# Performance work log

Hardware: AMD Instinct MI355X
Metric: run time of the kernel (lower is better)

The kernel has to match this reference:

```python
import jax, jax.numpy as jnp
import numpy as np

B, C, H, W = 16, 96, 64, 64
N = H * W
BN = B * N
K = 16  # neighbors per node
E = BN * K
C_OUT = 96


def setup_inputs() -> dict:
    key = jax.random.key(0)
    k1, k2, k3, k4 = jax.random.split(key, 4)
    x = jax.random.normal(k1, (B, C, H, W), dtype=jnp.float32)
    # KNN-style edge list over flat node ids (node = b*N + n):
    # every node appears K times as a target (row 0), random sources (row 1).
    dst = jnp.repeat(jnp.arange(BN, dtype=jnp.int64), K)
    src = jax.random.randint(k2, (E,), 0, BN, dtype=jnp.int64)
    edge_index = jnp.stack([dst, src], axis=0)
    Wc = jax.random.normal(k3, (C_OUT, 2 * C), dtype=jnp.float32) * 0.05
    bc = jax.random.normal(k4, (C_OUT,), dtype=jnp.float32) * 0.05
    return {"x": x, "edge_index": edge_index, "Wc": Wc, "bc": bc}


def reference(x, edge_index, Wc, bc):
    b, c, h, w = x.shape
    n = h * w
    # Flatten to node features [B*N, C] with node id = b*N + n
    feats = x.reshape(b, c, n).transpose(0, 2, 1).reshape(b * n, c)
    # Max-relative aggregation: gather, subtract, scatter-max over targets
    diff = feats[edge_index[1]] - feats[edge_index[0]]        # [E, C]
    agg = jax.ops.segment_max(diff, edge_index[0], num_segments=b * n)  # [BN, C]
    x_j = agg.reshape(b, n, c).transpose(0, 2, 1)             # [B, C, N]
    x_n = x.reshape(b, c, n)                                   # [B, C, N]
    # Interleaved channel concat: (x_0, xj_0, x_1, xj_1, ...) -> [B, 2C, N]
    cat = jnp.stack([x_n, x_j], axis=2).reshape(b, 2 * c, n)
    # BasicConv: 1x1 conv (GEMM over channels) + bias + ReLU
    out = jnp.einsum('oc,bcn->bon', Wc, cat) + bc[None, :, None]
    out = jax.nn.relu(out)
    return out.reshape(b, -1, h, w)
```

## Files before the change

kernel.cpp:

```cpp
#include <hip/hip_runtime.h>

#define B_   16
#define C_   96
#define N_   4096
#define BN_  65536
#define K_   16
#define E_   (BN_ * K_)

typedef __attribute__((ext_vector_type(8))) short bf16x8;
typedef __attribute__((ext_vector_type(4))) float f32x4;

union FragU { uint32_t u[4]; bf16x8 v; };

__device__ __forceinline__ uint32_t pack2_bf16(float a, float b) {
    uint32_t ua = __builtin_bit_cast(uint32_t, a);
    uint32_t ub = __builtin_bit_cast(uint32_t, b);
    ua = (ua + 0x7fffu + ((ua >> 16) & 1u)) >> 16;
    ub = (ub + 0x7fffu + ((ub >> 16) & 1u)) >> 16;
    return (ua & 0xffffu) | (ub << 16);
}
__device__ __forceinline__ float lo16f(uint32_t u) {
    return __builtin_bit_cast(float, u << 16);
}
__device__ __forceinline__ float hi16f(uint32_t u) {
    return __builtin_bit_cast(float, u & 0xffff0000u);
}

__global__ __launch_bounds__(256) void transpose_k(const float* __restrict__ x,
                                                   ushort* __restrict__ feats_bf) {
    __shared__ float tile[32][65];
    int b  = blockIdx.z;
    int c0 = blockIdx.y * 32;
    int n0 = blockIdx.x * 64;
    const float* xp = x + (size_t)b * C_ * N_;
    for (int t = threadIdx.x; t < 32 * 64; t += 256) {
        int c = t >> 6, n = t & 63;
        tile[c][n] = xp[(size_t)(c0 + c) * N_ + n0 + n];
    }
    __syncthreads();
    ushort* fp = feats_bf + ((size_t)b * N_ + n0) * C_ + c0;
    for (int t = threadIdx.x; t < 64 * 16; t += 256) {
        int n = t >> 4, cq = t & 15;
        uint32_t p = pack2_bf16(tile[2 * cq][n], tile[2 * cq + 1][n]);
        *(uint32_t*)(fp + (size_t)n * C_ + 2 * cq) = p;
    }
}

__global__ __launch_bounds__(256) void gather_max_k(const ushort* __restrict__ feats,
                                                    const int* __restrict__ src,
                                                    ushort* __restrict__ agg_bf) {
    int tid = threadIdx.x;
    int ln  = tid >> 3;
    int r   = tid & 7;
    size_t i = (size_t)blockIdx.x * 32 + ln;
    const int* s = src + i * K_;

    float m[12];
#pragma unroll
    for (int j = 0; j < 12; j++) m[j] = -3.0e38f;

#pragma unroll
    for (int q = 0; q < 4; q++) {
        int4 iv = ((const int4*)s)[q];
        int ids[4] = {iv.x, iv.y, iv.z, iv.w};
#pragma unroll
        for (int kk = 0; kk < 4; kk++) {
            const uint2* row = (const uint2*)(feats + (size_t)ids[kk] * C_);
#pragma unroll
            for (int j = 0; j < 3; j++) {
                uint2 v = row[r + 8 * j];
                m[4 * j + 0] = fmaxf(m[4 * j + 0], lo16f(v.x));
                m[4 * j + 1] = fmaxf(m[4 * j + 1], hi16f(v.x));
                m[4 * j + 2] = fmaxf(m[4 * j + 2], lo16f(v.y));
                m[4 * j + 3] = fmaxf(m[4 * j + 3], hi16f(v.y));
            }
        }
    }

    const uint2* own = (const uint2*)(feats + i * (size_t)C_);
    ushort* ap = agg_bf + i * (size_t)C_;
#pragma unroll
    for (int j = 0; j < 3; j++) {
        uint2 o = own[r + 8 * j];
        uint2 p;
        p.x = pack2_bf16(m[4 * j + 0] - lo16f(o.x), m[4 * j + 1] - hi16f(o.x));
        p.y = pack2_bf16(m[4 * j + 2] - lo16f(o.y), m[4 * j + 3] - hi16f(o.y));
        *(uint2*)(ap + (size_t)(r + 8 * j) * 4) = p;
    }
}

__global__ __launch_bounds__(256) void pack_w_k(const float* __restrict__ Wc,
                                                ushort* __restrict__ Wp) {
    int t = blockIdx.x * 256 + threadIdx.x;
    if (t >= 36 * 64) return;
    int fid = t >> 6, l = t & 63;
    int ks = fid / 6, to = fid % 6;
    int o = to * 16 + (l & 15), g = l >> 4;
    uint32_t packed[4];
#pragma unroll
    for (int h = 0; h < 4; h++) {
        int e0 = 2 * h, e1 = 2 * h + 1;
        int k0 = ks * 32 + 4 * g + (e0 & 3) + 16 * (e0 >> 2);
        int k1 = ks * 32 + 4 * g + (e1 & 3) + 16 * (e1 >> 2);
        int ko0 = (k0 < 96) ? 2 * k0 : 2 * (k0 - 96) + 1;
        int ko1 = (k1 < 96) ? 2 * k1 : 2 * (k1 - 96) + 1;
        packed[h] = pack2_bf16(Wc[(size_t)o * 192 + ko0], Wc[(size_t)o * 192 + ko1]);
    }
    uint4 u = make_uint4(packed[0], packed[1], packed[2], packed[3]);
    ((uint4*)Wp)[t] = u;
}

__global__ __launch_bounds__(256) void conv_mfma_k(const ushort* __restrict__ feats_bf,
                                                   const ushort* __restrict__ agg_bf,
                                                   const ushort* __restrict__ Wp,
                                                   const float* __restrict__ bc,
                                                   float* __restrict__ out) {
    __shared__ ushort A_lds[128 * 200];
    int tid = threadIdx.x;
    int w = tid >> 6, l = tid & 63;
    int blk = blockIdx.x;
    int b = blk >> 5;
    int n0 = (blk & 31) << 7;

    float bcr[6];
#pragma unroll
    for (int to = 0; to < 6; to++) bcr[to] = bc[to * 16 + (l & 15)];

    const ushort* fb = feats_bf + ((size_t)b * N_ + n0) * C_;
#pragma unroll
    for (int i = 0; i < 12; i++) {
        int tau = i * 256 + tid;
        int n = tau / 24;
        int q = tau - n * 24;
        uint2 p = *(const uint2*)(fb + (size_t)n * C_ + 4 * q);
        int idx = n * 200 + ((4 * q) ^ ((n & 15) << 2));
        *(uint2*)&A_lds[idx] = p;
    }
    const ushort* ab = agg_bf + ((size_t)b * N_ + n0) * C_;
#pragma unroll
    for (int i = 0; i < 12; i++) {
        int tau = i * 256 + tid;
        int n = tau / 24;
        int q = tau - n * 24;
        uint2 p = *(const uint2*)(ab + (size_t)n * C_ + 4 * q);
        int idx = n * 200 + ((96 + 4 * q) ^ ((n & 15) << 2));
        *(uint2*)&A_lds[idx] = p;
    }
    __syncthreads();

    f32x4 acc[2][6];
#pragma unroll
    for (int tm = 0; tm < 2; tm++)
#pragma unroll
        for (int to = 0; to < 6; to++)
            acc[tm][to] = (f32x4){0.f, 0.f, 0.f, 0.f};

    const uint4* wp4 = (const uint4*)Wp;
    int g = l >> 4;
    int m = (l & 15) << 2;

#pragma unroll
    for (int ks = 0; ks < 6; ks++) {
        FragU bfrag[6];
#pragma unroll
        for (int to = 0; to < 6; to++) {
            uint4 u = wp4[(ks * 6 + to) * 64 + l];
            bfrag[to].u[0] = u.x; bfrag[to].u[1] = u.y;
            bfrag[to].u[2] = u.z; bfrag[to].u[3] = u.w;
        }
        FragU afrag[2];
#pragma unroll
        for (int tm = 0; tm < 2; tm++) {
            int n = w * 32 + tm * 16 + (l & 15);
            int base = n * 200;
            int k1 = ks * 32 + 4 * g;
            uint2 lo = *(const uint2*)&A_lds[base + (k1 ^ m)];
            uint2 hi = *(const uint2*)&A_lds[base + ((k1 + 16) ^ m)];
            afrag[tm].u[0] = lo.x; afrag[tm].u[1] = lo.y;
            afrag[tm].u[2] = hi.x; afrag[tm].u[3] = hi.y;
        }
#pragma unroll
        for (int tm = 0; tm < 2; tm++)
#pragma unroll
            for (int to = 0; to < 6; to++)
                acc[tm][to] = __builtin_amdgcn_mfma_f32_16x16x32_bf16(
                    afrag[tm].v, bfrag[to].v, acc[tm][to], 0, 0, 0);
    }

    __syncthreads();
    float* OT = (float*)A_lds;
#pragma unroll
    for (int tm = 0; tm < 2; tm++)
#pragma unroll
        for (int to = 0; to < 6; to++) {
            int o = to * 16 + (l & 15);
#pragma unroll
            for (int reg = 0; reg < 4; reg++) {
                int nl = w * 32 + tm * 16 + ((l >> 4) << 2) + reg;
                OT[o * 132 + nl] = fmaxf(acc[tm][to][reg] + bcr[to], 0.0f);
            }
        }
    __syncthreads();

#pragma unroll
    for (int i = 0; i < 12; i++) {
        int f = i * 256 + tid;
        int o = f >> 5, c4 = f & 31;
        float4 v = *(const float4*)&OT[o * 132 + 4 * c4];
        *(float4*)(out + ((size_t)b * C_ + o) * N_ + n0 + 4 * c4) = v;
    }
}

extern "C" void kernel_launch(void* const* d_in, const int* in_sizes, int n_in,
                              void* d_out, int out_size, void* d_ws, size_t ws_size,
                              hipStream_t stream) {
    const float* x   = (const float*)d_in[0];
    const int*   ei  = (const int*)d_in[1];
    const float* Wc  = (const float*)d_in[2];
    const float* bc  = (const float*)d_in[3];
    float* out = (float*)d_out;

    const int* src = ei + E_;

    ushort* feats_bf = (ushort*)d_ws;
    ushort* agg_bf   = (ushort*)((char*)d_ws + (size_t)BN_ * C_ * 2);
    ushort* Wp       = (ushort*)((char*)d_ws + (size_t)BN_ * C_ * 4);

    pack_w_k<<<9, 256, 0, stream>>>(Wc, Wp);

    dim3 gA(N_ / 64, C_ / 32, B_);
    transpose_k<<<gA, 256, 0, stream>>>(x, feats_bf);

    gather_max_k<<<BN_ / 32, 256, 0, stream>>>(feats_bf, src, agg_bf);

    conv_mfma_k<<<B_ * (N_ / 128), 256, 0, stream>>>(feats_bf, agg_bf, Wp, bc, out);
}
```

Baseline: 59.20 us.

## Fold weight packing into gather kernel and simplify conv epilogue with 512 threads

The weight-packing kernel is merged into the gather-max launch as 9 extra tail blocks, which removes one kernel launch. The conv kernel moves to 512 threads with one 16-row M tile per wave. It loads its feature and aggregate tiles with 16-byte loads into an equivalent XOR-swizzled LDS layout. Its output is now written straight from registers as float4 stores, skipping the LDS transpose and two barriers, at the cost of less coalesced global writes (16-byte pieces strided by N).

```diff
diff --git a/kernel.cpp b/kernel.cpp
--- a/kernel.cpp
+++ b/kernel.cpp
@@ -48,8 +48,31 @@
 
 __global__ __launch_bounds__(256) void gather_max_k(const ushort* __restrict__ feats,
                                                     const int* __restrict__ src,
-                                                    ushort* __restrict__ agg_bf) {
+                                                    ushort* __restrict__ agg_bf,
+                                                    const float* __restrict__ Wc,
+                                                    ushort* __restrict__ Wp) {
     int tid = threadIdx.x;
+    if (blockIdx.x >= 2048) {
+        int t = (blockIdx.x - 2048) * 256 + tid;
+        if (t >= 36 * 64) return;
+        int fid = t >> 6, l = t & 63;
+        int ks = fid / 6, to = fid % 6;
+        int o = to * 16 + (l & 15), g = l >> 4;
+        uint32_t packed[4];
+#pragma unroll
+        for (int h = 0; h < 4; h++) {
+            int e0 = 2 * h, e1 = 2 * h + 1;
+            int k0 = ks * 32 + 4 * g + (e0 & 3) + 16 * (e0 >> 2);
+            int k1 = ks * 32 + 4 * g + (e1 & 3) + 16 * (e1 >> 2);
+            int ko0 = (k0 < 96) ? 2 * k0 : 2 * (k0 - 96) + 1;
+            int ko1 = (k1 < 96) ? 2 * k1 : 2 * (k1 - 96) + 1;
+            packed[h] = pack2_bf16(Wc[(size_t)o * 192 + ko0],
+                                   Wc[(size_t)o * 192 + ko1]);
+        }
+        ((uint4*)Wp)[t] = make_uint4(packed[0], packed[1], packed[2], packed[3]);
+        return;
+    }
+
     int ln  = tid >> 3;
     int r   = tid & 7;
     size_t i = (size_t)blockIdx.x * 32 + ln;
@@ -89,28 +112,7 @@
     }
 }
 
-__global__ __launch_bounds__(256) void pack_w_k(const float* __restrict__ Wc,
-                                                ushort* __restrict__ Wp) {
-    int t = blockIdx.x * 256 + threadIdx.x;
-    if (t >= 36 * 64) return;
-    int fid = t >> 6, l = t & 63;
-    int ks = fid / 6, to = fid % 6;
-    int o = to * 16 + (l & 15), g = l >> 4;
-    uint32_t packed[4];
-#pragma unroll
-    for (int h = 0; h < 4; h++) {
-        int e0 = 2 * h, e1 = 2 * h + 1;
-        int k0 = ks * 32 + 4 * g + (e0 & 3) + 16 * (e0 >> 2);
-        int k1 = ks * 32 + 4 * g + (e1 & 3) + 16 * (e1 >> 2);
-        int ko0 = (k0 < 96) ? 2 * k0 : 2 * (k0 - 96) + 1;
-        int ko1 = (k1 < 96) ? 2 * k1 : 2 * (k1 - 96) + 1;
-        packed[h] = pack2_bf16(Wc[(size_t)o * 192 + ko0], Wc[(size_t)o * 192 + ko1]);
-    }
-    uint4 u = make_uint4(packed[0], packed[1], packed[2], packed[3]);
-    ((uint4*)Wp)[t] = u;
-}
-
-__global__ __launch_bounds__(256) void conv_mfma_k(const ushort* __restrict__ feats_bf,
+__global__ __launch_bounds__(512) void conv_mfma_k(const ushort* __restrict__ feats_bf,
                                                    const ushort* __restrict__ agg_bf,
                                                    const ushort* __restrict__ Wp,
                                                    const float* __restrict__ bc,
@@ -127,37 +129,30 @@
     for (int to = 0; to < 6; to++) bcr[to] = bc[to * 16 + (l & 15)];
 
     const ushort* fb = feats_bf + ((size_t)b * N_ + n0) * C_;
-#pragma unroll
-    for (int i = 0; i < 12; i++) {
-        int tau = i * 256 + tid;
+    const ushort* ab = agg_bf + ((size_t)b * N_ + n0) * C_;
+#pragma unroll
+    for (int i = 0; i < 6; i++) {
+        int tau = i * 512 + tid;
         int n = tau / 24;
-        int q = tau - n * 24;
-        uint2 p = *(const uint2*)(fb + (size_t)n * C_ + 4 * q);
-        int idx = n * 200 + ((4 * q) ^ ((n & 15) << 2));
-        *(uint2*)&A_lds[idx] = p;
-    }
-    const ushort* ab = agg_bf + ((size_t)b * N_ + n0) * C_;
-#pragma unroll
-    for (int i = 0; i < 12; i++) {
-        int tau = i * 256 + tid;
-        int n = tau / 24;
-        int q = tau - n * 24;
-        uint2 p = *(const uint2*)(ab + (size_t)n * C_ + 4 * q);
-        int idx = n * 200 + ((96 + 4 * q) ^ ((n & 15) << 2));
-        *(uint2*)&A_lds[idx] = p;
+        int p = tau - n * 24;
+        const ushort* srcp = (p < 12) ? (fb + (size_t)n * C_ + 8 * p)
+                                      : (ab + (size_t)n * C_ + 8 * (p - 12));
+        uint4 u = *(const uint4*)srcp;
+        if (n & 1) { uint32_t t0 = u.x, t1 = u.y; u.x = u.z; u.y = u.w; u.z = t0; u.w = t1; }
+        int slot = p ^ ((n >> 1) & 7);
+        *(uint4*)&A_lds[n * 200 + slot * 8] = u;
     }
     __syncthreads();
 
-    f32x4 acc[2][6];
-#pragma unroll
-    for (int tm = 0; tm < 2; tm++)
-#pragma unroll
-        for (int to = 0; to < 6; to++)
-            acc[tm][to] = (f32x4){0.f, 0.f, 0.f, 0.f};
+    f32x4 acc[6];
+#pragma unroll
+    for (int to = 0; to < 6; to++) acc[to] = (f32x4){0.f, 0.f, 0.f, 0.f};
 
     const uint4* wp4 = (const uint4*)Wp;
     int g = l >> 4;
     int m = (l & 15) << 2;
+    int nrow = w * 16 + (l & 15);
+    int abase = nrow * 200;
 
 #pragma unroll
     for (int ks = 0; ks < 6; ks++) {
@@ -168,46 +163,28 @@
             bfrag[to].u[0] = u.x; bfrag[to].u[1] = u.y;
             bfrag[to].u[2] = u.z; bfrag[to].u[3] = u.w;
         }
-        FragU afrag[2];
-#pragma unroll
-        for (int tm = 0; tm < 2; tm++) {
-            int n = w * 32 + tm * 16 + (l & 15);
-            int base = n * 200;
-            int k1 = ks * 32 + 4 * g;
-            uint2 lo = *(const uint2*)&A_lds[base + (k1 ^ m)];
-            uint2 hi = *(const uint2*)&A_lds[base + ((k1 + 16) ^ m)];
-            afrag[tm].u[0] = lo.x; afrag[tm].u[1] = lo.y;
-            afrag[tm].u[2] = hi.x; afrag[tm].u[3] = hi.y;
-        }
-#pragma unroll
-        for (int tm = 0; tm < 2; tm++)
-#pragma unroll
-            for (int to = 0; to < 6; to++)
-                acc[tm][to] = __builtin_amdgcn_mfma_f32_16x16x32_bf16(
-                    afrag[tm].v, bfrag[to].v, acc[tm][to], 0, 0, 0);
-    }
-
-    __syncthreads();
-    float* OT = (float*)A_lds;
-#pragma unroll
-    for (int tm = 0; tm < 2; tm++)
-#pragma unroll
-        for (int to = 0; to < 6; to++) {
-            int o = to * 16 + (l & 15);
-#pragma unroll
-            for (int reg = 0; reg < 4; reg++) {
-                int nl = w * 32 + tm * 16 + ((l >> 4) << 2) + reg;
-                OT[o * 132 + nl] = fmaxf(acc[tm][to][reg] + bcr[to], 0.0f);
-            }
-        }
-    __syncthreads();
-
-#pragma unroll
-    for (int i = 0; i < 12; i++) {
-        int f = i * 256 + tid;
-        int o = f >> 5, c4 = f & 31;
-        float4 v = *(const float4*)&OT[o * 132 + 4 * c4];
-        *(float4*)(out + ((size_t)b * C_ + o) * N_ + n0 + 4 * c4) = v;
+        int k1 = ks * 32 + 4 * g;
+        uint2 lo = *(const uint2*)&A_lds[abase + (k1 ^ m)];
+        uint2 hi = *(const uint2*)&A_lds[abase + ((k1 + 16) ^ m)];
+        FragU afrag;
+        afrag.u[0] = lo.x; afrag.u[1] = lo.y;
+        afrag.u[2] = hi.x; afrag.u[3] = hi.y;
+#pragma unroll
+        for (int to = 0; to < 6; to++)
+            acc[to] = __builtin_amdgcn_mfma_f32_16x16x32_bf16(
+                afrag.v, bfrag[to].v, acc[to], 0, 0, 0);
+    }
+
+    int nl = n0 + w * 16 + ((l >> 4) << 2);
+#pragma unroll
+    for (int to = 0; to < 6; to++) {
+        int o = to * 16 + (l & 15);
+        float4 v;
+        v.x = fmaxf(acc[to][0] + bcr[to], 0.0f);
+        v.y = fmaxf(acc[to][1] + bcr[to], 0.0f);
+        v.z = fmaxf(acc[to][2] + bcr[to], 0.0f);
+        v.w = fmaxf(acc[to][3] + bcr[to], 0.0f);
+        *(float4*)(out + ((size_t)b * C_ + o) * N_ + nl) = v;
     }
 }
 
@@ -226,12 +203,10 @@
     ushort* agg_bf   = (ushort*)((char*)d_ws + (size_t)BN_ * C_ * 2);
     ushort* Wp       = (ushort*)((char*)d_ws + (size_t)BN_ * C_ * 4);
 
-    pack_w_k<<<9, 256, 0, stream>>>(Wc, Wp);
-
     dim3 gA(N_ / 64, C_ / 32, B_);
     transpose_k<<<gA, 256, 0, stream>>>(x, feats_bf);
 
-    gather_max_k<<<BN_ / 32, 256, 0, stream>>>(feats_bf, src, agg_bf);
-
-    conv_mfma_k<<<B_ * (N_ / 128), 256, 0, stream>>>(feats_bf, agg_bf, Wp, bc, out);
-}
+    gather_max_k<<<2057, 256, 0, stream>>>(feats_bf, src, agg_bf, Wc, Wp);
+
+    conv_mfma_k<<<B_ * (N_ / 128), 512, 0, stream>>>(feats_bf, agg_bf, Wp, bc, out);
+}
```

After: 57.01 us. -3.7%, faster.
